# Performance work log

Measured on AMD Instinct MI355X. Metric: run time of the kernel, lower is better.

The kernel has to match this reference:

```python
import jax, jax.numpy as jnp
import numpy as np

EPS = 1e-5  # torch default eps for both LayerNorm and BatchNorm
NH, KD, HD = 8, 16, 32  # num_heads, key_dim, head_dim for inc=256


def conv1x1(x, w, b=None):
    # w: [Cout, Cin]; x: [B, Cin, H, W]
    y = jnp.einsum('oc,bchw->bohw', w, x)
    return y if b is None else y + b[None, :, None, None]


def dwconv3x3(x, w, b=None):
    # depthwise 3x3, padding 1; w: [C, 1, 3, 3]
    C = x.shape[1]
    y = jax.lax.conv_general_dilated(x, w, (1, 1), ((1, 1), (1, 1)),
                                     dimension_numbers=('NCHW', 'OIHW', 'NCHW'),
                                     feature_group_count=C)
    return y if b is None else y + b[None, :, None, None]


def bn_eval(x, p):
    # p: [4, C] stacked (gamma, beta, running_mean, running_var); eval-mode BN
    g, b, m, v = p
    s = (g * jax.lax.rsqrt(v + EPS))[None, :, None, None]
    return (x - m[None, :, None, None]) * s + b[None, :, None, None]


def ln2d(x, g, b):
    # LayerNorm over channel dim (== permute->LN(C)->permute in torch)
    mu = x.mean(axis=1, keepdims=True)
    var = x.var(axis=1, keepdims=True)  # biased var, matches F.layer_norm
    return (x - mu) * jax.lax.rsqrt(var + EPS) * g[None, :, None, None] + b[None, :, None, None]


def setup_inputs() -> dict:
    key = jax.random.key(0)
    ks = jax.random.split(key, 20)
    B, C, H, W = 8, 256, 32, 32
    h_qkv = C + 2 * NH * KD  # 512
    hid = int(2 * C / 3)     # 170

    def bn_params(k, c):
        k1, k2, k3, k4 = jax.random.split(k, 4)
        g = 1.0 + 0.1 * jax.random.normal(k1, (c,), jnp.float32)
        b = 0.1 * jax.random.normal(k2, (c,), jnp.float32)
        m = 0.1 * jax.random.normal(k3, (c,), jnp.float32)
        v = jax.random.uniform(k4, (c,), jnp.float32, 0.5, 1.5)
        return jnp.stack([g, b, m, v])

    sc = lambda fan: 1.0 / np.sqrt(fan)
    return {
        'x': jax.random.normal(ks[0], (B, C, H, W), jnp.float32),
        'ln1_g': 1.0 + 0.1 * jax.random.normal(ks[1], (C,), jnp.float32),
        'ln1_b': 0.1 * jax.random.normal(ks[2], (C,), jnp.float32),
        'ln2_g': 1.0 + 0.1 * jax.random.normal(ks[3], (C,), jnp.float32),
        'ln2_b': 0.1 * jax.random.normal(ks[4], (C,), jnp.float32),
        'qkv_w': sc(C) * jax.random.normal(ks[5], (h_qkv, C), jnp.float32),
        'qkv_bn': bn_params(ks[6], h_qkv),
        'pe_w': sc(9) * jax.random.normal(ks[7], (C, 1, 3, 3), jnp.float32),
        'pe_bn': bn_params(ks[8], C),
        'proj_w': sc(C) * jax.random.normal(ks[9], (C, C), jnp.float32),
        'proj_bn': bn_params(ks[10], C),
        'fc1_w': sc(C) * jax.random.normal(ks[11], (2 * hid, C), jnp.float32),
        'fc1_b': 0.01 * jax.random.normal(ks[12], (2 * hid,), jnp.float32),
        'dw_w': sc(9) * jax.random.normal(ks[13], (hid, 1, 3, 3), jnp.float32),
        'dw_b': 0.01 * jax.random.normal(ks[14], (hid,), jnp.float32),
        'fc2_w': sc(hid) * jax.random.normal(ks[15], (C, hid), jnp.float32),
        'fc2_b': 0.01 * jax.random.normal(ks[16], (C,), jnp.float32),
    }


def reference(x, ln1_g, ln1_b, ln2_g, ln2_b, qkv_w, qkv_bn, pe_w, pe_bn,
              proj_w, proj_bn, fc1_w, fc1_b, dw_w, dw_b, fc2_w, fc2_b):
    B, C, H, W = x.shape
    N = H * W

    # --- PSA attention branch (eval mode: drop_path = identity) ---
    xn = ln2d(x, ln1_g, ln1_b)
    qkv = bn_eval(conv1x1(xn, qkv_w), qkv_bn)            # [B, 2*nh*kd + C, H, W]
    qkv = qkv.reshape(B, NH, 2 * KD + HD, N)
    q, k, v = qkv[:, :, :KD], qkv[:, :, KD:2 * KD], qkv[:, :, 2 * KD:]
    scale = KD ** -0.5
    attn = jax.nn.softmax(jnp.einsum('bhkn,bhkm->bhnm', q, k) * scale, axis=-1)
    o = jnp.einsum('bhdm,bhnm->bhdn', v, attn).reshape(B, C, H, W)
    o = o + bn_eval(dwconv3x3(v.reshape(B, C, H, W), pe_w), pe_bn)
    o = bn_eval(conv1x1(o, proj_w), proj_bn)
    x = x + o

    # --- Convolutional GLU branch (internal residual uses normed input) ---
    xn2 = ln2d(x, ln2_g, ln2_b)
    h = conv1x1(xn2, fc1_w, fc1_b)
    a, g = jnp.split(h, 2, axis=1)
    a = jax.nn.gelu(dwconv3x3(a, dw_w, dw_b), approximate=False) * g
    mlp_out = xn2 + conv1x1(a, fc2_w, fc2_b)
    return x + mlp_out
```

## Files before the change

kernel.cpp:

```cpp
#include <hip/hip_runtime.h>
#include <hip/hip_bf16.h>
#include <math.h>

#define EPSF 1e-5f

using short2v = __attribute__((ext_vector_type(2))) short;
using short4v = __attribute__((ext_vector_type(4))) short;
using short8 = __attribute__((ext_vector_type(8))) short;
using f32x4 = __attribute__((ext_vector_type(4))) float;

__device__ inline short bfbits(float x) {
  __hip_bfloat16 h = __float2bfloat16(x);
  return __builtin_bit_cast(short, h);
}
__device__ inline float bf2f(short s) {
  unsigned u = ((unsigned)(unsigned short)s) << 16;
  return __builtin_bit_cast(float, u);
}

__global__ __launch_bounds__(256) void prep_kernel(
    const float* __restrict__ qkv_w, const float* __restrict__ qkv_bn,
    const float* __restrict__ proj_w, const float* __restrict__ proj_bn,
    const float* __restrict__ fc1_w, const float* __restrict__ fc2_w,
    const float* __restrict__ pe_w, const float* __restrict__ pe_bn,
    const float* __restrict__ dw_w, const float* __restrict__ dw_b,
    short* __restrict__ wq, float* __restrict__ bq, short* __restrict__ wpj,
    float* __restrict__ bpj, short* __restrict__ wf1, short* __restrict__ wf2,
    float* __restrict__ pwT, float* __restrict__ pbv, float* __restrict__ wdT,
    float* __restrict__ dbv) {
  int id = blockIdx.x * 256 + threadIdx.x;
  if (id < 131072) {
    int o = id >> 8, k = id & 255;
    float g = qkv_bn[o], bb = qkv_bn[512 + o], m = qkv_bn[1024 + o],
          v = qkv_bn[1536 + o];
    float s = g * rsqrtf(v + EPSF);
    float s2 = ((o & 63) < 16) ? 0.25f : 1.0f;
    wq[id] = bfbits(qkv_w[id] * s * s2);
    if (k == 0) bq[o] = (bb - m * s) * s2;
  } else if (id < 196608) {
    int i = id - 131072;
    int o = i >> 8, k = i & 255;
    float g = proj_bn[o], bb = proj_bn[256 + o], m = proj_bn[512 + o],
          v = proj_bn[768 + o];
    float s = g * rsqrtf(v + EPSF);
    wpj[i] = bfbits(proj_w[i] * s);
    if (k == 0) bpj[o] = bb - m * s;
  } else if (id < 294912) {
    int i = id - 196608;
    int o = i >> 8, k = i & 255;
    wf1[i] = bfbits(o < 340 ? fc1_w[o * 256 + k] : 0.f);
  } else if (id < 344064) {
    int i = id - 294912;
    int o = i / 192, k = i - o * 192;
    wf2[i] = bfbits(k < 170 ? fc2_w[o * 170 + k] : 0.f);
  } else if (id < 346368) {
    int i = id - 344064;
    int c = i & 255, tap = i >> 8;
    float g = pe_bn[c], bb = pe_bn[256 + c], m = pe_bn[512 + c],
          v = pe_bn[768 + c];
    float s = g * rsqrtf(v + EPSF);
    pwT[tap * 256 + c] = pe_w[c * 9 + tap] * s;
    if (tap == 0) pbv[c] = bb - m * s;
  } else if (id < 348096) {
    int i = id - 346368;
    int c = i % 192, tap = i / 192;
    wdT[tap * 192 + c] = (c < 170) ? dw_w[c * 9 + tap] : 0.f;
    if (tap == 0) dbv[c] = (c < 170) ? dw_b[c] : 0.f;
  }
}

__global__ __launch_bounds__(256) void ln1_kernel(
    const float* __restrict__ x, const float* __restrict__ gamma,
    const float* __restrict__ beta, short* __restrict__ xn) {
  __shared__ float s_sum[16][16];
  __shared__ float s_sq[16][16];
  int t = threadIdx.x;
  int nl = t & 15, cg = t >> 4;
  int p0 = blockIdx.x * 16;
  int b = p0 >> 10;
  int n = (p0 & 1023) + nl;
  const float* xp = x + ((size_t)b * 256 + cg * 16) * 1024 + n;
  float v[16];
  float sum = 0.f, sq = 0.f;
#pragma unroll
  for (int i = 0; i < 16; ++i) {
    float val = xp[(size_t)i * 1024];
    v[i] = val;
    sum += val;
    sq += val * val;
  }
  s_sum[cg][nl] = sum;
  s_sq[cg][nl] = sq;
  __syncthreads();
  float ts = 0.f, tq = 0.f;
#pragma unroll
  for (int g = 0; g < 16; ++g) {
    ts += s_sum[g][nl];
    tq += s_sq[g][nl];
  }
  float mu = ts * (1.f / 256.f);
  float var = tq * (1.f / 256.f) - mu * mu;
  float rs = rsqrtf(var + EPSF);
  short8 pk[2];
#pragma unroll
  for (int i = 0; i < 16; ++i) {
    int c = cg * 16 + i;
    pk[i >> 3][i & 7] = bfbits((v[i] - mu) * rs * gamma[c] + beta[c]);
  }
  short* op = xn + ((size_t)b * 1024 + n) * 256 + cg * 16;
  *reinterpret_cast<short8*>(op) = pk[0];
  *reinterpret_cast<short8*>(op + 8) = pk[1];
}

__global__ __launch_bounds__(256) void ln2_kernel(
    const float* __restrict__ x1, const float* __restrict__ gamma,
    const float* __restrict__ beta, short* __restrict__ xn2) {
  int t = threadIdx.x;
  int lane = t & 63, w = t >> 6;
  f32x4 gv = *reinterpret_cast<const f32x4*>(&gamma[lane * 4]);
  f32x4 bv = *reinterpret_cast<const f32x4*>(&beta[lane * 4]);
#pragma unroll
  for (int it = 0; it < 4; ++it) {
    size_t pos = blockIdx.x * 16 + w * 4 + it;
    f32x4 xv = *reinterpret_cast<const f32x4*>(&x1[pos * 256 + lane * 4]);
    float s = (xv[0] + xv[1]) + (xv[2] + xv[3]);
    float q = (xv[0] * xv[0] + xv[1] * xv[1]) + (xv[2] * xv[2] + xv[3] * xv[3]);
#pragma unroll
    for (int off = 1; off < 64; off <<= 1) {
      s += __shfl_xor(s, off);
      q += __shfl_xor(q, off);
    }
    float mu = s * (1.f / 256.f);
    float var = q * (1.f / 256.f) - mu * mu;
    float rs = rsqrtf(var + EPSF);
    short4v o;
#pragma unroll
    for (int e = 0; e < 4; ++e)
      o[e] = bfbits((xv[e] - mu) * rs * gv[e] + bv[e]);
    *reinterpret_cast<short4v*>(&xn2[pos * 256 + lane * 4]) = o;
  }
}

template <int MODE>
__global__ __launch_bounds__(256) void gemm3_kernel(
    const short* __restrict__ X, const short* __restrict__ W,
    const float* __restrict__ bias, const float* __restrict__ addCM,
    const float* __restrict__ add1CL, const short* __restrict__ add2CL,
    void* __restrict__ out, int OC, int K, int OT, int KS, int RS) {
  __shared__ short Wl[128][40];
  __shared__ short Xl[64][40];
  int bx = blockIdx.x;
  int ot = bx % OT;
  int ntb = bx / OT;
  int b = ntb >> 4;
  int n0 = (ntb & 15) * 64;
  int o0 = ot * 128;
  int t = threadIdx.x;
  int lane = t & 63, w = t >> 6;
  int wo = w >> 1, wn = w & 1;
  int g = lane >> 4, r = lane & 15;
  int srow = t >> 2, sk8 = (t & 3) * 8;
  size_t bN = (size_t)b * 1024;
  const short* Wp0 = W + (size_t)(o0 + srow) * K + sk8;
  const short* Wp1 = W + (size_t)(o0 + 64 + srow) * K + sk8;
  const short* Xp = X + (bN + n0 + srow) * KS + sk8;
  f32x4 acc[4][2] = {};
  int nsteps = K >> 5;
  short8 w0 = *reinterpret_cast<const short8*>(Wp0);
  short8 w1 = *reinterpret_cast<const short8*>(Wp1);
  short8 x0 = *reinterpret_cast<const short8*>(Xp);
  for (int ks = 0; ks < nsteps; ++ks) {
    *reinterpret_cast<short8*>(&Wl[srow][sk8]) = w0;
    *reinterpret_cast<short8*>(&Wl[64 + srow][sk8]) = w1;
    *reinterpret_cast<short8*>(&Xl[srow][sk8]) = x0;
    __syncthreads();
    if (ks + 1 < nsteps) {
      int ko = (ks + 1) << 5;
      w0 = *reinterpret_cast<const short8*>(Wp0 + ko);
      w1 = *reinterpret_cast<const short8*>(Wp1 + ko);
      x0 = *reinterpret_cast<const short8*>(Xp + ko);
    }
    short8 a[4], bb[2];
#pragma unroll
    for (int i = 0; i < 4; ++i)
      a[i] = *reinterpret_cast<const short8*>(&Wl[wo * 64 + i * 16 + r][g * 8]);
#pragma unroll
    for (int j = 0; j < 2; ++j)
      bb[j] = *reinterpret_cast<const short8*>(&Xl[wn * 32 + j * 16 + r][g * 8]);
#pragma unroll
    for (int i = 0; i < 4; ++i)
#pragma unroll
      for (int j = 0; j < 2; ++j)
        acc[i][j] = __builtin_amdgcn_mfma_f32_16x16x32_bf16(a[i], bb[j],
                                                            acc[i][j], 0, 0, 0);
    __syncthreads();
  }
#pragma unroll
  for (int i = 0; i < 4; ++i) {
#pragma unroll
    for (int j = 0; j < 2; ++j) {
      int oq = o0 + wo * 64 + i * 16 + g * 4;
      if (oq >= OC) continue;
      int n = n0 + wn * 32 + j * 16 + r;
      f32x4 bv = *reinterpret_cast<const f32x4*>(&bias[oq]);
      f32x4 res;
#pragma unroll
      for (int rr = 0; rr < 4; ++rr) res[rr] = acc[i][j][rr] + bv[rr];
      if constexpr (MODE == 0) {
        short4v s;
#pragma unroll
        for (int rr = 0; rr < 4; ++rr) s[rr] = bfbits(res[rr]);
        *reinterpret_cast<short4v*>((short*)out + (bN + n) * RS + oq) = s;
      } else if constexpr (MODE == 1) {
#pragma unroll
        for (int rr = 0; rr < 4; ++rr)
          res[rr] += addCM[((size_t)b * 256 + oq + rr) * 1024 + n];
        *reinterpret_cast<f32x4*>((float*)out + (bN + n) * 256 + oq) = res;
      } else {
        f32x4 a1v = *reinterpret_cast<const f32x4*>(&add1CL[(bN + n) * 256 + oq]);
        short4v a2v = *reinterpret_cast<const short4v*>(&add2CL[(bN + n) * 256 + oq]);
#pragma unroll
        for (int rr = 0; rr < 4; ++rr) {
          float v = res[rr] + a1v[rr] + bf2f(a2v[rr]);
          ((float*)out)[((size_t)b * 256 + oq + rr) * 1024 + n] = v;
        }
      }
    }
  }
}

__global__ __launch_bounds__(256) void attn3_kernel(
    const short* __restrict__ qkv, const float* __restrict__ pwT,
    const float* __restrict__ pbv, short* __restrict__ obf) {
  __shared__ short Ql[64][40];
  __shared__ short Kl[64][40];
  __shared__ short Vl[32][72];
  __shared__ short Ol[64][36];
  int blk = blockIdx.x;
  int qt = blk & 15, h = (blk >> 4) & 7, b = blk >> 7;
  size_t bN = (size_t)b * 1024;
  const short* base = qkv + bN * 512 + h * 64;
  int t = threadIdx.x;
  int lane = t & 63, w = t >> 6;
  int g = lane >> 4, r = lane & 15;
  int q0 = qt * 64;
  for (int i = t; i < 64 * 16; i += 256) {
    int row = i >> 4, col = 16 + (i & 15);
    Ql[row][col] = 0;
    Kl[row][col] = 0;
  }
  {
    int qr = t >> 2, kd4 = (t & 3) * 4;
    short4v qv =
        *reinterpret_cast<const short4v*>(&base[(size_t)(q0 + qr) * 512 + kd4]);
    *reinterpret_cast<short4v*>(&Ql[qr][kd4]) = qv;
  }
  __syncthreads();
  short8 qf = *reinterpret_cast<const short8*>(&Ql[w * 16 + r][g * 8]);
  float M = -3e38f, l = 0.f;
  f32x4 O0 = {}, O1 = {};
  int mr4 = t >> 2, kd4 = (t & 3) * 4;
  int mp = t & 31, dq8 = t >> 5;
  short4v kreg =
      *reinterpret_cast<const short4v*>(&base[(size_t)mr4 * 512 + 16 + kd4]);
  short4v vA = *reinterpret_cast<const short4v*>(
      &base[(size_t)(2 * mp) * 512 + 32 + dq8 * 4]);
  short4v vB = *reinterpret_cast<const short4v*>(
      &base[(size_t)(2 * mp + 1) * 512 + 32 + dq8 * 4]);
  for (int ch = 0; ch < 16; ++ch) {
    *reinterpret_cast<short4v*>(&Kl[mr4][kd4]) = kreg;
#pragma unroll
    for (int e = 0; e < 4; ++e) {
      short2v p = {vA[e], vB[e]};
      *reinterpret_cast<short2v*>(&Vl[dq8 * 4 + e][2 * mp]) = p;
    }
    __syncthreads();
    if (ch + 1 < 16) {
      int m0 = (ch + 1) * 64;
      kreg = *reinterpret_cast<const short4v*>(
          &base[(size_t)(m0 + mr4) * 512 + 16 + kd4]);
      vA = *reinterpret_cast<const short4v*>(
          &base[(size_t)(m0 + 2 * mp) * 512 + 32 + dq8 * 4]);
      vB = *reinterpret_cast<const short4v*>(
          &base[(size_t)(m0 + 2 * mp + 1) * 512 + 32 + dq8 * 4]);
    }
    f32x4 s4[4];
#pragma unroll
    for (int mt = 0; mt < 4; ++mt) {
      short8 af = *reinterpret_cast<const short8*>(&Kl[mt * 16 + r][g * 8]);
      f32x4 z = {};
      s4[mt] = __builtin_amdgcn_mfma_f32_16x16x32_bf16(af, qf, z, 0, 0, 0);
    }
    float mx = -3e38f;
#pragma unroll
    for (int mt = 0; mt < 4; ++mt)
      mx = fmaxf(mx,
                 fmaxf(fmaxf(s4[mt][0], s4[mt][1]), fmaxf(s4[mt][2], s4[mt][3])));
    mx = fmaxf(mx, __shfl_xor(mx, 16));
    mx = fmaxf(mx, __shfl_xor(mx, 32));
    float Mn = fmaxf(M, mx);
    float f = __expf(M - Mn);
    M = Mn;
    float sc = 0.f;
    short8 pa[4];
#pragma unroll
    for (int mt = 0; mt < 4; ++mt) {
      float p0 = __expf(s4[mt][0] - Mn);
      float p1 = __expf(s4[mt][1] - Mn);
      float p2 = __expf(s4[mt][2] - Mn);
      float p3 = __expf(s4[mt][3] - Mn);
      sc += (p0 + p1) + (p2 + p3);
      pa[mt] = (short8){bfbits(p0), bfbits(p1), bfbits(p2), bfbits(p3),
                        0, 0, 0, 0};
    }
    sc += __shfl_xor(sc, 16);
    sc += __shfl_xor(sc, 32);
    l = l * f + sc;
#pragma unroll
    for (int rr = 0; rr < 4; ++rr) {
      float fr = __shfl(f, g * 4 + rr);
      O0[rr] *= fr;
      O1[rr] *= fr;
    }
#pragma unroll
    for (int mt = 0; mt < 4; ++mt) {
      short4v v0 = *reinterpret_cast<const short4v*>(&Vl[r][mt * 16 + g * 4]);
      short4v v1 =
          *reinterpret_cast<const short4v*>(&Vl[16 + r][mt * 16 + g * 4]);
      short8 b0 = {v0[0], v0[1], v0[2], v0[3], 0, 0, 0, 0};
      short8 b1 = {v1[0], v1[1], v1[2], v1[3], 0, 0, 0, 0};
      O0 = __builtin_amdgcn_mfma_f32_16x16x32_bf16(pa[mt], b0, O0, 0, 0, 0);
      O1 = __builtin_amdgcn_mfma_f32_16x16x32_bf16(pa[mt], b1, O1, 0, 0, 0);
    }
    __syncthreads();
  }
#pragma unroll
  for (int rr = 0; rr < 4; ++rr) {
    float lr = __shfl(l, g * 4 + rr);
    float inv = 1.f / lr;
    int q = w * 16 + g * 4 + rr;
    Ol[q][r] = bfbits(O0[rr] * inv);
    Ol[q][16 + r] = bfbits(O1[rr] * inv);
  }
  __syncthreads();
#pragma unroll
  for (int it = 0; it < 2; ++it) {
    int item = t + it * 256;
    int q = item & 63, dq = item >> 6;
    int n = q0 + q;
    int y = n >> 5, xx = n & 31;
    int cq = h * 32 + dq * 4;
    f32x4 s = *reinterpret_cast<const f32x4*>(&pbv[cq]);
#pragma unroll
    for (int dy = -1; dy <= 1; ++dy) {
      int yy = y + dy;
      if (yy < 0 || yy > 31) continue;
#pragma unroll
      for (int dx = -1; dx <= 1; ++dx) {
        int xw = xx + dx;
        if (xw < 0 || xw > 31) continue;
        int tap = (dy + 1) * 3 + (dx + 1);
        f32x4 wv = *reinterpret_cast<const f32x4*>(&pwT[tap * 256 + cq]);
        short4v vv = *reinterpret_cast<const short4v*>(
            &base[(size_t)(yy * 32 + xw) * 512 + 32 + dq * 4]);
#pragma unroll
        for (int e = 0; e < 4; ++e) s[e] += wv[e] * bf2f(vv[e]);
      }
    }
    short4v ov = *reinterpret_cast<const short4v*>(&Ol[q][dq * 4]);
    short4v res;
#pragma unroll
    for (int e = 0; e < 4; ++e) res[e] = bfbits(bf2f(ov[e]) + s[e]);
    *reinterpret_cast<short4v*>(&obf[(bN + n) * 256 + cq]) = res;
  }
}

__global__ __launch_bounds__(256) void glu3_kernel(
    const short* __restrict__ h, const float* __restrict__ wdT,
    const float* __restrict__ dbv, short* __restrict__ act) {
  int t = threadIdx.x;
  int pos = blockIdx.x * 16 + (t >> 4);
  int c0 = (t & 15) * 12;
  int n = pos & 1023;
  int b = pos >> 10;
  int y = n >> 5, xx = n & 31;
  const short* hb = h + (size_t)b * 1024 * 352;
  float s[12];
#pragma unroll
  for (int e = 0; e < 12; ++e) s[e] = dbv[c0 + e];
#pragma unroll
  for (int dy = -1; dy <= 1; ++dy) {
    int yy = y + dy;
    if (yy < 0 || yy > 31) continue;
#pragma unroll
    for (int dx = -1; dx <= 1; ++dx) {
      int xw = xx + dx;
      if (xw < 0 || xw > 31) continue;
      int tap = (dy + 1) * 3 + (dx + 1);
      const float* wp = wdT + tap * 192 + c0;
      const short* ap = hb + (size_t)(yy * 32 + xw) * 352 + c0;
#pragma unroll
      for (int v4 = 0; v4 < 3; ++v4) {
        short4v av = *reinterpret_cast<const short4v*>(ap + v4 * 4);
        f32x4 wv = *reinterpret_cast<const f32x4*>(wp + v4 * 4);
#pragma unroll
        for (int e = 0; e < 4; ++e) s[v4 * 4 + e] += wv[e] * bf2f(av[e]);
      }
    }
  }
  const short* gp = hb + (size_t)n * 352 + 170 + c0;
  short* arow = act + ((size_t)b * 1024 + n) * 192 + c0;
#pragma unroll
  for (int v4 = 0; v4 < 3; ++v4) {
    short4v res;
#pragma unroll
    for (int e = 0; e < 4; ++e) {
      float sv = s[v4 * 4 + e];
      float ge = 0.5f * sv * (1.f + erff(sv * 0.70710678118654752f));
      res[e] = bfbits(ge * bf2f(gp[v4 * 4 + e]));
    }
    *reinterpret_cast<short4v*>(arow + v4 * 4) = res;
  }
}

extern "C" void kernel_launch(void* const* d_in, const int* in_sizes, int n_in,
                              void* d_out, int out_size, void* d_ws,
                              size_t ws_size, hipStream_t stream) {
  const float* x      = (const float*)d_in[0];
  const float* ln1_g  = (const float*)d_in[1];
  const float* ln1_b  = (const float*)d_in[2];
  const float* ln2_g  = (const float*)d_in[3];
  const float* ln2_b  = (const float*)d_in[4];
  const float* qkv_w  = (const float*)d_in[5];
  const float* qkv_bn = (const float*)d_in[6];
  const float* pe_w   = (const float*)d_in[7];
  const float* pe_bn  = (const float*)d_in[8];
  const float* proj_w = (const float*)d_in[9];
  const float* proj_bn= (const float*)d_in[10];
  const float* fc1_w  = (const float*)d_in[11];
  const float* fc1_b  = (const float*)d_in[12];
  const float* dw_w   = (const float*)d_in[13];
  const float* dw_b   = (const float*)d_in[14];
  const float* fc2_w  = (const float*)d_in[15];
  const float* fc2_b  = (const float*)d_in[16];

  char* base = (char*)d_ws;
  short* xn   = (short*)(base + 0);
  short* qkv  = (short*)(base + 4194304);
  short* obf  = (short*)(base + 12582912);
  float* x1   = (float*)(base + 16777216);
  short* xn2  = (short*)(base + 25165824);
  short* hbuf = (short*)(base + 29360128);
  short* act  = (short*)(base + 35131392);
  short* wq   = (short*)(base + 38277120);
  short* wpj  = (short*)(base + 38539264);
  short* wf1  = (short*)(base + 38670336);
  short* wf2  = (short*)(base + 38866944);
  float* pwT  = (float*)(base + 38965248);
  float* pbv  = (float*)(base + 38974464);
  float* wdT  = (float*)(base + 38975488);
  float* dbv  = (float*)(base + 38982400);
  float* bq   = (float*)(base + 38983168);
  float* bpj  = (float*)(base + 38985216);
  float* outp = (float*)d_out;

  hipLaunchKernelGGL(prep_kernel, dim3(1360), dim3(256), 0, stream, qkv_w,
                     qkv_bn, proj_w, proj_bn, fc1_w, fc2_w, pe_w, pe_bn, dw_w,
                     dw_b, wq, bq, wpj, bpj, wf1, wf2, pwT, pbv, wdT, dbv);
  hipLaunchKernelGGL(ln1_kernel, dim3(512), dim3(256), 0, stream, x, ln1_g,
                     ln1_b, xn);
  hipLaunchKernelGGL((gemm3_kernel<0>), dim3(512), dim3(256), 0, stream, xn,
                     wq, bq, nullptr, nullptr, nullptr, qkv, 512, 256, 4, 256,
                     512);
  hipLaunchKernelGGL(attn3_kernel, dim3(1024), dim3(256), 0, stream, qkv, pwT,
                     pbv, obf);
  hipLaunchKernelGGL((gemm3_kernel<1>), dim3(256), dim3(256), 0, stream, obf,
                     wpj, bpj, x, nullptr, nullptr, x1, 256, 256, 2, 256, 256);
  hipLaunchKernelGGL(ln2_kernel, dim3(512), dim3(256), 0, stream, x1, ln2_g,
                     ln2_b, xn2);
  hipLaunchKernelGGL((gemm3_kernel<0>), dim3(384), dim3(256), 0, stream, xn2,
                     wf1, fc1_b, nullptr, nullptr, nullptr, hbuf, 340, 256, 3,
                     256, 352);
  hipLaunchKernelGGL(glu3_kernel, dim3(512), dim3(256), 0, stream, hbuf, wdT,
                     dbv, act);
  hipLaunchKernelGGL((gemm3_kernel<2>), dim3(256), dim3(256), 0, stream, act,
                     wf2, fc2_b, nullptr, x1, xn2, outp, 256, 192, 2, 192,
                     256);
}
```

Baseline: 182.6 us.

## Double-buffer attention K/V, lazy softmax rescale, exp2 scaling, deeper GEMM K-step

The attention kernel now double-buffers K/V tiles in LDS, so the next chunk is stored after the current one is used and one barrier per iteration goes away. Online softmax skips the max update and the O rescale unless some row's max grows by more than a threshold. Exponentials use exp2f with log2(e) folded into the Q weights, and the block index order now iterates heads fastest. The GEMM moves from a 32-wide to a 64-wide K step per LDS stage, halving the loop trips and barriers at the cost of more LDS and registers; the deferred rescale also risks overflow headroom if the threshold logic is wrong.

```diff
diff --git a/kernel.cpp b/kernel.cpp
--- a/kernel.cpp
+++ b/kernel.cpp
@@ -34,7 +34,7 @@
     float g = qkv_bn[o], bb = qkv_bn[512 + o], m = qkv_bn[1024 + o],
           v = qkv_bn[1536 + o];
     float s = g * rsqrtf(v + EPSF);
-    float s2 = ((o & 63) < 16) ? 0.25f : 1.0f;
+    float s2 = ((o & 63) < 16) ? 0.25f * 1.44269504088896f : 1.0f;
     wq[id] = bfbits(qkv_w[id] * s * s2);
     if (k == 0) bq[o] = (bb - m * s) * s2;
   } else if (id < 196608) {
@@ -142,13 +142,13 @@
 }
 
 template <int MODE>
-__global__ __launch_bounds__(256) void gemm3_kernel(
+__global__ __launch_bounds__(256) void gemm4_kernel(
     const short* __restrict__ X, const short* __restrict__ W,
     const float* __restrict__ bias, const float* __restrict__ addCM,
     const float* __restrict__ add1CL, const short* __restrict__ add2CL,
     void* __restrict__ out, int OC, int K, int OT, int KS, int RS) {
-  __shared__ short Wl[128][40];
-  __shared__ short Xl[64][40];
+  __shared__ short Wl[128][72];
+  __shared__ short Xl[64][72];
   int bx = blockIdx.x;
   int ot = bx % OT;
   int ntb = bx / OT;
@@ -159,40 +159,55 @@
   int lane = t & 63, w = t >> 6;
   int wo = w >> 1, wn = w & 1;
   int g = lane >> 4, r = lane & 15;
-  int srow = t >> 2, sk8 = (t & 3) * 8;
+  int rw = t >> 1, cw = (t & 1) * 32;
+  int rx = t >> 2, cx = (t & 3) * 16;
   size_t bN = (size_t)b * 1024;
-  const short* Wp0 = W + (size_t)(o0 + srow) * K + sk8;
-  const short* Wp1 = W + (size_t)(o0 + 64 + srow) * K + sk8;
-  const short* Xp = X + (bN + n0 + srow) * KS + sk8;
+  const short* Wp = W + (size_t)(o0 + rw) * K + cw;
+  const short* Xp = X + (bN + n0 + rx) * KS + cx;
   f32x4 acc[4][2] = {};
-  int nsteps = K >> 5;
-  short8 w0 = *reinterpret_cast<const short8*>(Wp0);
-  short8 w1 = *reinterpret_cast<const short8*>(Wp1);
-  short8 x0 = *reinterpret_cast<const short8*>(Xp);
+  int nsteps = K >> 6;
+  short8 wreg[4], xreg[2];
+#pragma unroll
+  for (int e = 0; e < 4; ++e)
+    wreg[e] = *reinterpret_cast<const short8*>(Wp + e * 8);
+#pragma unroll
+  for (int e = 0; e < 2; ++e)
+    xreg[e] = *reinterpret_cast<const short8*>(Xp + e * 8);
   for (int ks = 0; ks < nsteps; ++ks) {
-    *reinterpret_cast<short8*>(&Wl[srow][sk8]) = w0;
-    *reinterpret_cast<short8*>(&Wl[64 + srow][sk8]) = w1;
-    *reinterpret_cast<short8*>(&Xl[srow][sk8]) = x0;
+#pragma unroll
+    for (int e = 0; e < 4; ++e)
+      *reinterpret_cast<short8*>(&Wl[rw][cw + e * 8]) = wreg[e];
+#pragma unroll
+    for (int e = 0; e < 2; ++e)
+      *reinterpret_cast<short8*>(&Xl[rx][cx + e * 8]) = xreg[e];
     __syncthreads();
     if (ks + 1 < nsteps) {
-      int ko = (ks + 1) << 5;
-      w0 = *reinterpret_cast<const short8*>(Wp0 + ko);
-      w1 = *reinterpret_cast<const short8*>(Wp1 + ko);
-      x0 = *reinterpret_cast<const short8*>(Xp + ko);
-    }
-    short8 a[4], bb[2];
-#pragma unroll
-    for (int i = 0; i < 4; ++i)
-      a[i] = *reinterpret_cast<const short8*>(&Wl[wo * 64 + i * 16 + r][g * 8]);
-#pragma unroll
-    for (int j = 0; j < 2; ++j)
-      bb[j] = *reinterpret_cast<const short8*>(&Xl[wn * 32 + j * 16 + r][g * 8]);
-#pragma unroll
-    for (int i = 0; i < 4; ++i)
+      int ko = (ks + 1) << 6;
+#pragma unroll
+      for (int e = 0; e < 4; ++e)
+        wreg[e] = *reinterpret_cast<const short8*>(Wp + ko + e * 8);
+#pragma unroll
+      for (int e = 0; e < 2; ++e)
+        xreg[e] = *reinterpret_cast<const short8*>(Xp + ko + e * 8);
+    }
+#pragma unroll
+    for (int kk = 0; kk < 2; ++kk) {
+      short8 a[4], bb[2];
+#pragma unroll
+      for (int i = 0; i < 4; ++i)
+        a[i] = *reinterpret_cast<const short8*>(
+            &Wl[wo * 64 + i * 16 + r][kk * 32 + g * 8]);
 #pragma unroll
       for (int j = 0; j < 2; ++j)
-        acc[i][j] = __builtin_amdgcn_mfma_f32_16x16x32_bf16(a[i], bb[j],
-                                                            acc[i][j], 0, 0, 0);
+        bb[j] = *reinterpret_cast<const short8*>(
+            &Xl[wn * 32 + j * 16 + r][kk * 32 + g * 8]);
+#pragma unroll
+      for (int i = 0; i < 4; ++i)
+#pragma unroll
+        for (int j = 0; j < 2; ++j)
+          acc[i][j] = __builtin_amdgcn_mfma_f32_16x16x32_bf16(
+              a[i], bb[j], acc[i][j], 0, 0, 0);
+    }
     __syncthreads();
   }
 #pragma unroll
@@ -229,15 +244,15 @@
   }
 }
 
-__global__ __launch_bounds__(256) void attn3_kernel(
+__global__ __launch_bounds__(256) void attn4_kernel(
     const short* __restrict__ qkv, const float* __restrict__ pwT,
     const float* __restrict__ pbv, short* __restrict__ obf) {
   __shared__ short Ql[64][40];
-  __shared__ short Kl[64][40];
-  __shared__ short Vl[32][72];
+  __shared__ short Kl[2][64][40];
+  __shared__ short Vl[2][32][72];
   __shared__ short Ol[64][36];
   int blk = blockIdx.x;
-  int qt = blk & 15, h = (blk >> 4) & 7, b = blk >> 7;
+  int h = blk & 7, qt = (blk >> 3) & 15, b = blk >> 7;
   size_t bN = (size_t)b * 1024;
   const short* base = qkv + bN * 512 + h * 64;
   int t = threadIdx.x;
@@ -247,7 +262,8 @@
   for (int i = t; i < 64 * 16; i += 256) {
     int row = i >> 4, col = 16 + (i & 15);
     Ql[row][col] = 0;
-    Kl[row][col] = 0;
+    Kl[0][row][col] = 0;
+    Kl[1][row][col] = 0;
   }
   {
     int qr = t >> 2, kd4 = (t & 3) * 4;
@@ -255,10 +271,6 @@
         *reinterpret_cast<const short4v*>(&base[(size_t)(q0 + qr) * 512 + kd4]);
     *reinterpret_cast<short4v*>(&Ql[qr][kd4]) = qv;
   }
-  __syncthreads();
-  short8 qf = *reinterpret_cast<const short8*>(&Ql[w * 16 + r][g * 8]);
-  float M = -3e38f, l = 0.f;
-  f32x4 O0 = {}, O1 = {};
   int mr4 = t >> 2, kd4 = (t & 3) * 4;
   int mp = t & 31, dq8 = t >> 5;
   short4v kreg =
@@ -267,14 +279,18 @@
       &base[(size_t)(2 * mp) * 512 + 32 + dq8 * 4]);
   short4v vB = *reinterpret_cast<const short4v*>(
       &base[(size_t)(2 * mp + 1) * 512 + 32 + dq8 * 4]);
+  *reinterpret_cast<short4v*>(&Kl[0][mr4][kd4]) = kreg;
+#pragma unroll
+  for (int e = 0; e < 4; ++e) {
+    short2v p = {vA[e], vB[e]};
+    *reinterpret_cast<short2v*>(&Vl[0][dq8 * 4 + e][2 * mp]) = p;
+  }
+  __syncthreads();
+  short8 qf = *reinterpret_cast<const short8*>(&Ql[w * 16 + r][g * 8]);
+  float M = -3e38f, l = 0.f;
+  f32x4 O0 = {}, O1 = {};
   for (int ch = 0; ch < 16; ++ch) {
-    *reinterpret_cast<short4v*>(&Kl[mr4][kd4]) = kreg;
-#pragma unroll
-    for (int e = 0; e < 4; ++e) {
-      short2v p = {vA[e], vB[e]};
-      *reinterpret_cast<short2v*>(&Vl[dq8 * 4 + e][2 * mp]) = p;
-    }
-    __syncthreads();
+    int cur = ch & 1;
     if (ch + 1 < 16) {
       int m0 = (ch + 1) * 64;
       kreg = *reinterpret_cast<const short4v*>(
@@ -287,28 +303,29 @@
     f32x4 s4[4];
 #pragma unroll
     for (int mt = 0; mt < 4; ++mt) {
-      short8 af = *reinterpret_cast<const short8*>(&Kl[mt * 16 + r][g * 8]);
+      short8 af = *reinterpret_cast<const short8*>(&Kl[cur][mt * 16 + r][g * 8]);
       f32x4 z = {};
       s4[mt] = __builtin_amdgcn_mfma_f32_16x16x32_bf16(af, qf, z, 0, 0, 0);
     }
-    float mx = -3e38f;
+    float pm = -3e38f;
 #pragma unroll
     for (int mt = 0; mt < 4; ++mt)
-      mx = fmaxf(mx,
+      pm = fmaxf(pm,
                  fmaxf(fmaxf(s4[mt][0], s4[mt][1]), fmaxf(s4[mt][2], s4[mt][3])));
-    mx = fmaxf(mx, __shfl_xor(mx, 16));
-    mx = fmaxf(mx, __shfl_xor(mx, 32));
-    float Mn = fmaxf(M, mx);
-    float f = __expf(M - Mn);
+    pm = fmaxf(pm, __shfl_xor(pm, 16));
+    pm = fmaxf(pm, __shfl_xor(pm, 32));
+    bool full = !__all(pm - M <= 8.f);
+    float Mn = full ? fmaxf(M, pm) : M;
+    float f = full ? exp2f(M - Mn) : 1.f;
     M = Mn;
     float sc = 0.f;
     short8 pa[4];
 #pragma unroll
     for (int mt = 0; mt < 4; ++mt) {
-      float p0 = __expf(s4[mt][0] - Mn);
-      float p1 = __expf(s4[mt][1] - Mn);
-      float p2 = __expf(s4[mt][2] - Mn);
-      float p3 = __expf(s4[mt][3] - Mn);
+      float p0 = exp2f(s4[mt][0] - Mn);
+      float p1 = exp2f(s4[mt][1] - Mn);
+      float p2 = exp2f(s4[mt][2] - Mn);
+      float p3 = exp2f(s4[mt][3] - Mn);
       sc += (p0 + p1) + (p2 + p3);
       pa[mt] = (short8){bfbits(p0), bfbits(p1), bfbits(p2), bfbits(p3),
                         0, 0, 0, 0};
@@ -316,21 +333,32 @@
     sc += __shfl_xor(sc, 16);
     sc += __shfl_xor(sc, 32);
     l = l * f + sc;
-#pragma unroll
-    for (int rr = 0; rr < 4; ++rr) {
-      float fr = __shfl(f, g * 4 + rr);
-      O0[rr] *= fr;
-      O1[rr] *= fr;
+    if (full) {
+#pragma unroll
+      for (int rr = 0; rr < 4; ++rr) {
+        float fr = __shfl(f, g * 4 + rr);
+        O0[rr] *= fr;
+        O1[rr] *= fr;
+      }
     }
 #pragma unroll
     for (int mt = 0; mt < 4; ++mt) {
-      short4v v0 = *reinterpret_cast<const short4v*>(&Vl[r][mt * 16 + g * 4]);
+      short4v v0 = *reinterpret_cast<const short4v*>(&Vl[cur][r][mt * 16 + g * 4]);
       short4v v1 =
-          *reinterpret_cast<const short4v*>(&Vl[16 + r][mt * 16 + g * 4]);
+          *reinterpret_cast<const short4v*>(&Vl[cur][16 + r][mt * 16 + g * 4]);
       short8 b0 = {v0[0], v0[1], v0[2], v0[3], 0, 0, 0, 0};
       short8 b1 = {v1[0], v1[1], v1[2], v1[3], 0, 0, 0, 0};
       O0 = __builtin_amdgcn_mfma_f32_16x16x32_bf16(pa[mt], b0, O0, 0, 0, 0);
       O1 = __builtin_amdgcn_mfma_f32_16x16x32_bf16(pa[mt], b1, O1, 0, 0, 0);
+    }
+    if (ch + 1 < 16) {
+      int nxt = cur ^ 1;
+      *reinterpret_cast<short4v*>(&Kl[nxt][mr4][kd4]) = kreg;
+#pragma unroll
+      for (int e = 0; e < 4; ++e) {
+        short2v p = {vA[e], vB[e]};
+        *reinterpret_cast<short2v*>(&Vl[nxt][dq8 * 4 + e][2 * mp]) = p;
+      }
     }
     __syncthreads();
   }
@@ -469,21 +497,21 @@
                      dw_b, wq, bq, wpj, bpj, wf1, wf2, pwT, pbv, wdT, dbv);
   hipLaunchKernelGGL(ln1_kernel, dim3(512), dim3(256), 0, stream, x, ln1_g,
                      ln1_b, xn);
-  hipLaunchKernelGGL((gemm3_kernel<0>), dim3(512), dim3(256), 0, stream, xn,
+  hipLaunchKernelGGL((gemm4_kernel<0>), dim3(512), dim3(256), 0, stream, xn,
                      wq, bq, nullptr, nullptr, nullptr, qkv, 512, 256, 4, 256,
                      512);
-  hipLaunchKernelGGL(attn3_kernel, dim3(1024), dim3(256), 0, stream, qkv, pwT,
+  hipLaunchKernelGGL(attn4_kernel, dim3(1024), dim3(256), 0, stream, qkv, pwT,
                      pbv, obf);
-  hipLaunchKernelGGL((gemm3_kernel<1>), dim3(256), dim3(256), 0, stream, obf,
+  hipLaunchKernelGGL((gemm4_kernel<1>), dim3(256), dim3(256), 0, stream, obf,
                      wpj, bpj, x, nullptr, nullptr, x1, 256, 256, 2, 256, 256);
   hipLaunchKernelGGL(ln2_kernel, dim3(512), dim3(256), 0, stream, x1, ln2_g,
                      ln2_b, xn2);
-  hipLaunchKernelGGL((gemm3_kernel<0>), dim3(384), dim3(256), 0, stream, xn2,
+  hipLaunchKernelGGL((gemm4_kernel<0>), dim3(384), dim3(256), 0, stream, xn2,
                      wf1, fc1_b, nullptr, nullptr, nullptr, hbuf, 340, 256, 3,
                      256, 352);
   hipLaunchKernelGGL(glu3_kernel, dim3(512), dim3(256), 0, stream, hbuf, wdT,
                      dbv, act);
-  hipLaunchKernelGGL((gemm3_kernel<2>), dim3(256), dim3(256), 0, stream, act,
+  hipLaunchKernelGGL((gemm4_kernel<2>), dim3(256), dim3(256), 0, stream, act,
                      wf2, fc2_b, nullptr, x1, xn2, outp, 256, 192, 2, 192,
                      256);
 }
```

Measured after the change: 177.6 us. 1.03x faster.
